# Optimization experiments

Hardware: AMD Instinct MI355X
Metric: run time of the kernel (lower is better)

Reference implementation:

```python
import jax, jax.numpy as jnp
import numpy as np

D_MODEL = 1024
NUM_HEADS = 16
D_HEAD = D_MODEL // NUM_HEADS
THETA = 10000.0


def _apply_rope(x, pos):
    # x: [B, H, S, Dh]; pos: [S]
    inv_freq = 1.0 / (THETA ** (jnp.arange(0, D_HEAD, 2, dtype=jnp.float32) / D_HEAD))  # [Dh/2]
    freqs = pos[:, None].astype(x.dtype) * inv_freq.astype(x.dtype)  # [S, Dh/2]
    cos = jnp.cos(freqs)  # [S, Dh/2]
    sin = jnp.sin(freqs)
    x1 = x[..., 0::2]  # [B, H, S, Dh/2]
    x2 = x[..., 1::2]
    even = x1 * cos - x2 * sin
    odd = x1 * sin + x2 * cos
    # interleave back: stack on last axis then flatten
    out = jnp.stack([even, odd], axis=-1).reshape(x.shape)
    return out


def setup_inputs() -> dict:
    key = jax.random.key(0)
    k0, k1, k2, k3, k4 = jax.random.split(key, 5)
    B, S = 2, 2048
    scale = 0.02
    return {
        "in_features": jax.random.normal(k0, (B, S, D_MODEL), dtype=jnp.float32),
        "Wq": jax.random.normal(k1, (D_MODEL, D_MODEL), dtype=jnp.float32) * scale,
        "Wk": jax.random.normal(k2, (D_MODEL, D_MODEL), dtype=jnp.float32) * scale,
        "Wv": jax.random.normal(k3, (D_MODEL, D_MODEL), dtype=jnp.float32) * scale,
        "Wo": jax.random.normal(k4, (D_MODEL, D_MODEL), dtype=jnp.float32) * scale,
    }


def reference(in_features, Wq, Wk, Wv, Wo):
    B, S, _ = in_features.shape
    H, Dh = NUM_HEADS, D_HEAD

    def proj(W):
        # torch Linear: y = x @ W^T; split heads -> [B, H, S, Dh]
        y = jnp.einsum('bsd,ed->bse', in_features, W)
        return y.reshape(B, S, H, Dh).transpose(0, 2, 1, 3)

    q = proj(Wq)
    k = proj(Wk)
    v = proj(Wv)

    pos = jnp.arange(S)
    q = _apply_rope(q, pos)
    k = _apply_rope(k, pos)

    scores = jnp.einsum('bhqd,bhkd->bhqk', q, k) / jnp.sqrt(jnp.asarray(Dh, q.dtype))
    causal = jnp.tril(jnp.ones((S, S), dtype=bool))  # True = keep
    scores = jnp.where(causal[None, None, :, :], scores, -jnp.inf)
    att = jax.nn.softmax(scores, axis=-1)
    out = jnp.einsum('bhqk,bhkd->bhqd', att, v)  # [B, H, S, Dh]
    out = out.transpose(0, 2, 1, 3).reshape(B, S, H * Dh)
    return jnp.einsum('bsd,ed->bse', out, Wo)
```

## Files before the change

kernel.cpp:

```cpp
#include <hip/hip_runtime.h>
#include <hip/hip_bf16.h>
#include <math.h>

#define D_MODEL 1024
#define NHEAD 16
#define DHEAD 64
#define SEQ 2048
#define BATCH 2
#define MTOT (BATCH * SEQ)

typedef __attribute__((ext_vector_type(8))) short bf16x8;
typedef __attribute__((ext_vector_type(4))) float f32x4;

static __device__ __forceinline__ ushort f2b(float x) {
  __hip_bfloat16 h = __float2bfloat16(x);
  union { __hip_bfloat16 h; ushort u; } cv; cv.h = h; return cv.u;
}

#define GLLDS16(gp, lp)                                                     \
  __builtin_amdgcn_global_load_lds(                                         \
      (const __attribute__((address_space(1))) unsigned int*)(gp),          \
      (__attribute__((address_space(3))) unsigned int*)(lp), 16, 0, 0)

#define QSCALE 0.18033688011112042f

__global__ __launch_bounds__(256)
void prep(const float* __restrict__ X, const float* __restrict__ Wq,
          const float* __restrict__ Wk, const float* __restrict__ Wv,
          const float* __restrict__ Wo, ushort* __restrict__ Xb,
          ushort* __restrict__ Wqb, ushort* __restrict__ Wkb,
          ushort* __restrict__ Wvb, ushort* __restrict__ Wob,
          float2* __restrict__ tbl) {
  int bid = blockIdx.x;
  if (bid >= 8192) {
    int idx = (bid - 8192) * 256 + threadIdx.x;
    int s = idx >> 5, i = idx & 31;
    float inv = exp2f((float)i * -0.4152410118609203f);
    float sn, cs;
    sincosf((float)s * inv, &sn, &cs);
    tbl[idx] = make_float2(cs, sn);
    return;
  }
  const float* in;
  ushort* out;
  int i;
  if (bid < 4096) {
    in = X; out = Xb; i = bid * 256 + threadIdx.x;
  } else {
    int ws = (bid - 4096) >> 10;
    in = (ws == 0) ? Wq : (ws == 1) ? Wk : (ws == 2) ? Wv : Wo;
    out = (ws == 0) ? Wqb : (ws == 1) ? Wkb : (ws == 2) ? Wvb : Wob;
    i = ((bid - 4096) & 1023) * 256 + threadIdx.x;
  }
  float4 v = ((const float4*)in)[i];
  ushort4 o;
  o.x = f2b(v.x); o.y = f2b(v.y); o.z = f2b(v.z); o.w = f2b(v.w);
  ((ushort4*)out)[i] = o;
}

__global__ __launch_bounds__(256)
void gemm_bf16(const ushort* __restrict__ A,
               const ushort* __restrict__ W0, const ushort* __restrict__ W1,
               const ushort* __restrict__ W2,
               const float2* __restrict__ tbl,
               float* __restrict__ outF,
               ushort* __restrict__ o0, ushort* __restrict__ o1,
               ushort* __restrict__ o2, int mode) {
  __shared__ ushort As[128 * 32];
  __shared__ ushort Bs[128 * 32];
  const int tid = threadIdx.x;
  const int lane = tid & 63;
  const int w = tid >> 6;
  const int quad = lane >> 4, l15 = lane & 15;
  const int wy = w >> 1, wx = w & 1;
  const int m0 = blockIdx.y * 128, n0 = blockIdx.x * 128;
  const int z = blockIdx.z;
  const ushort* W = (z == 0) ? W0 : (z == 1) ? W1 : W2;
  ushort* outB = (z == 0) ? o0 : (z == 1) ? o1 : o2;

  const int r0 = tid >> 2, c0 = tid & 3;
  const int gc = c0 ^ (((r0 >> 2) ^ r0) & 3);
  const ushort* Ag0 = A + (size_t)(m0 + r0) * D_MODEL + gc * 8;
  const ushort* Ag1 = A + (size_t)(m0 + r0 + 64) * D_MODEL + gc * 8;
  const ushort* Wg0 = W + (size_t)(n0 + r0) * D_MODEL + gc * 8;
  const ushort* Wg1 = W + (size_t)(n0 + r0 + 64) * D_MODEL + gc * 8;

  const int sw = (quad ^ (l15 >> 2) ^ l15) & 3;

  f32x4 acc[4][4];
#pragma unroll
  for (int i = 0; i < 4; ++i)
#pragma unroll
    for (int j = 0; j < 4; ++j) acc[i][j] = (f32x4){0.f, 0.f, 0.f, 0.f};

  for (int kt = 0; kt < D_MODEL / 32; ++kt) {
    if (kt) __syncthreads();
    GLLDS16(Ag0 + kt * 32, &As[(size_t)tid * 8]);
    GLLDS16(Ag1 + kt * 32, &As[(size_t)(tid + 256) * 8]);
    GLLDS16(Wg0 + kt * 32, &Bs[(size_t)tid * 8]);
    GLLDS16(Wg1 + kt * 32, &Bs[(size_t)(tid + 256) * 8]);
    __syncthreads();

    bf16x8 af[4], bfr[4];
#pragma unroll
    for (int mt = 0; mt < 4; ++mt) {
      int row = wy * 64 + mt * 16 + l15;
      af[mt] = *(const bf16x8*)&As[(row * 4 + sw) * 8];
    }
#pragma unroll
    for (int nt = 0; nt < 4; ++nt) {
      int row = wx * 64 + nt * 16 + l15;
      bfr[nt] = *(const bf16x8*)&Bs[(row * 4 + sw) * 8];
    }
#pragma unroll
    for (int mt = 0; mt < 4; ++mt)
#pragma unroll
      for (int nt = 0; nt < 4; ++nt)
        acc[mt][nt] = __builtin_amdgcn_mfma_f32_16x16x32_bf16(
            af[mt], bfr[nt], acc[mt][nt], 0, 0, 0);
  }

  const float qsc = (z == 0) ? QSCALE : 1.0f;
#pragma unroll
  for (int mt = 0; mt < 4; ++mt) {
    int m_base = m0 + wy * 64 + mt * 16 + quad * 4;
    int b = m_base >> 11, s_base = m_base & (SEQ - 1);
#pragma unroll
    for (int nt = 0; nt < 4; ++nt) {
      int n = n0 + wx * 64 + nt * 16 + l15;
      if (mode == 0) {
#pragma unroll
        for (int r = 0; r < 4; ++r)
          outF[(size_t)(m_base + r) * D_MODEL + n] = acc[mt][nt][r];
      } else {
        int h = n >> 6, dh = n & 63;
        if (z == 2) {
          int p_base = (s_base & ~31) | (((s_base >> 2) & 3) << 3) |
                       (((s_base >> 4) & 1) << 2);
          ushort4 o;
          o.x = f2b(acc[mt][nt][0]); o.y = f2b(acc[mt][nt][1]);
          o.z = f2b(acc[mt][nt][2]); o.w = f2b(acc[mt][nt][3]);
          *(ushort4*)&outB[((size_t)(b * NHEAD + h) * DHEAD + dh) * SEQ + p_base] = o;
        } else {
          int i = nt * 8 + (l15 >> 1);
          bool evn = !(l15 & 1);
#pragma unroll
          for (int r = 0; r < 4; ++r) {
            float v = acc[mt][nt][r];
            float pv = __shfl_xor(v, 1);
            float2 csn = tbl[(s_base + r) * 32 + i];
            v = v * csn.x + (evn ? -pv * csn.y : pv * csn.y);
            v *= qsc;
            outB[(((size_t)(b * NHEAD + h)) * SEQ + s_base + r) * DHEAD + dh] = f2b(v);
          }
        }
      }
    }
  }
}

__global__ __launch_bounds__(256)
void flash_mfma(const ushort* __restrict__ Q, const ushort* __restrict__ K,
                const ushort* __restrict__ Vt, ushort* __restrict__ O) {
  __shared__ ushort Ks[64 * 64];
  __shared__ ushort Vs[64 * 64];
  const int tid = threadIdx.x;
  const int lane = tid & 63, w = tid >> 6;
  const int quad = lane >> 4, l15 = lane & 15;
  const int h = blockIdx.y, b = blockIdx.z;
  const int qt = (h >= 8) ? (31 - blockIdx.x) : blockIdx.x;
  const int bh = b * NHEAD + h;

  const int qrow = qt * 64 + w * 16 + l15;
  const ushort* Qrow = Q + ((size_t)bh * SEQ + qrow) * 64;
  bf16x8 aq0 = *(const bf16x8*)(Qrow + quad * 8);
  bf16x8 aq1 = *(const bf16x8*)(Qrow + 32 + quad * 8);

  const int rl = tid >> 3;
  const int gsc = (tid & 7) ^ (rl & 7);
  const ushort* Kg0 = K + ((size_t)bh * SEQ + rl) * 64 + gsc * 8;
  const ushort* Kg1 = Kg0 + (size_t)32 * 64;
  const ushort* Vg0 = Vt + ((size_t)bh * 64 + rl) * SEQ + gsc * 8;
  const ushort* Vg1 = Vg0 + (size_t)32 * SEQ;

  const int sA = (quad ^ (l15 & 7)) * 8;
  const int sB = sA ^ 32;

  float rsl = 0.f;
  f32x4 accO[4];
#pragma unroll
  for (int nt = 0; nt < 4; ++nt) accO[nt] = (f32x4){0.f, 0.f, 0.f, 0.f};

  float4 pk0 = *(const float4*)(Kg0);
  float4 pk1 = *(const float4*)(Kg1);
  float4 pv0 = *(const float4*)(Vg0);
  float4 pv1 = *(const float4*)(Vg1);

  for (int kt = 0; kt <= qt; ++kt) {
    __syncthreads();
    *(float4*)&Ks[tid * 8]        = pk0;
    *(float4*)&Ks[2048 + tid * 8] = pk1;
    *(float4*)&Vs[tid * 8]        = pv0;
    *(float4*)&Vs[2048 + tid * 8] = pv1;
    __syncthreads();
    if (kt < qt) {
      pk0 = *(const float4*)(Kg0 + (size_t)(kt + 1) * 64 * 64);
      pk1 = *(const float4*)(Kg1 + (size_t)(kt + 1) * 64 * 64);
      pv0 = *(const float4*)(Vg0 + (kt + 1) * 64);
      pv1 = *(const float4*)(Vg1 + (kt + 1) * 64);
    }

    f32x4 sc[4];
#pragma unroll
    for (int nt = 0; nt < 4; ++nt) {
      const ushort* kr = &Ks[(nt * 16 + l15) * 64];
      bf16x8 bk0 = *(const bf16x8*)(kr + sA);
      bf16x8 bk1 = *(const bf16x8*)(kr + sB);
      f32x4 zz = (f32x4){0.f, 0.f, 0.f, 0.f};
      zz = __builtin_amdgcn_mfma_f32_16x16x32_bf16(bk0, aq0, zz, 0, 0, 0);
      zz = __builtin_amdgcn_mfma_f32_16x16x32_bf16(bk1, aq1, zz, 0, 0, 0);
      sc[nt] = zz;
    }

    const bool diag = (kt == qt);
    uint pk[8];
#pragma unroll
    for (int nt = 0; nt < 4; ++nt) {
      int kbase = kt * 64 + nt * 16 + quad * 4;
      ushort us[4];
#pragma unroll
      for (int r = 0; r < 4; ++r) {
        float p = __builtin_amdgcn_exp2f(sc[nt][r]);
        if (diag && kbase + r > qrow) p = 0.f;
        rsl += p;
        us[r] = f2b(p);
      }
      pk[nt * 2]     = (uint)us[0] | ((uint)us[1] << 16);
      pk[nt * 2 + 1] = (uint)us[2] | ((uint)us[3] << 16);
    }
    union { uint u[4]; bf16x8 v; } B0, B1;
    B0.u[0] = pk[0]; B0.u[1] = pk[1]; B0.u[2] = pk[2]; B0.u[3] = pk[3];
    B1.u[0] = pk[4]; B1.u[1] = pk[5]; B1.u[2] = pk[6]; B1.u[3] = pk[7];

#pragma unroll
    for (int nt = 0; nt < 4; ++nt) {
      const ushort* vr = &Vs[(nt * 16 + l15) * 64];
      bf16x8 av0 = *(const bf16x8*)(vr + sA);
      bf16x8 av1 = *(const bf16x8*)(vr + sB);
      accO[nt] = __builtin_amdgcn_mfma_f32_16x16x32_bf16(av0, B0.v, accO[nt], 0, 0, 0);
      accO[nt] = __builtin_amdgcn_mfma_f32_16x16x32_bf16(av1, B1.v, accO[nt], 0, 0, 0);
    }
  }

  rsl += __shfl_xor(rsl, 16);
  rsl += __shfl_xor(rsl, 32);
  float invl = 1.f / rsl;

  size_t base = ((size_t)(b * SEQ + qrow)) * D_MODEL + h * 64;
#pragma unroll
  for (int nt = 0; nt < 4; ++nt) {
    ushort4 o;
    o.x = f2b(accO[nt][0] * invl);
    o.y = f2b(accO[nt][1] * invl);
    o.z = f2b(accO[nt][2] * invl);
    o.w = f2b(accO[nt][3] * invl);
    *(ushort4*)&O[base + nt * 16 + quad * 4] = o;
  }
}

extern "C" void kernel_launch(void* const* d_in, const int* in_sizes, int n_in,
                              void* d_out, int out_size, void* d_ws, size_t ws_size,
                              hipStream_t stream) {
  const float* X  = (const float*)d_in[0];
  const float* Wq = (const float*)d_in[1];
  const float* Wk = (const float*)d_in[2];
  const float* Wv = (const float*)d_in[3];
  const float* Wo = (const float*)d_in[4];
  float* out = (float*)d_out;

  ushort* Xb  = (ushort*)d_ws;
  ushort* Wqb = Xb  + (size_t)MTOT * D_MODEL;
  ushort* Wkb = Wqb + (size_t)D_MODEL * D_MODEL;
  ushort* Wvb = Wkb + (size_t)D_MODEL * D_MODEL;
  ushort* Wob = Wvb + (size_t)D_MODEL * D_MODEL;
  ushort* Qw  = Wob + (size_t)D_MODEL * D_MODEL;
  ushort* Kw  = Qw  + (size_t)MTOT * D_MODEL;
  ushort* Vtw = Kw  + (size_t)MTOT * D_MODEL;
  ushort* At  = Vtw + (size_t)MTOT * D_MODEL;
  float2* tbl = (float2*)(At + (size_t)MTOT * D_MODEL);

  prep<<<8448, 256, 0, stream>>>(X, Wq, Wk, Wv, Wo, Xb, Wqb, Wkb, Wvb, Wob, tbl);

  gemm_bf16<<<dim3(D_MODEL / 128, MTOT / 128, 3), 256, 0, stream>>>(
      Xb, Wqb, Wkb, Wvb, tbl, nullptr, Qw, Kw, Vtw, 1);

  flash_mfma<<<dim3(SEQ / 64, NHEAD, BATCH), 256, 0, stream>>>(Qw, Kw, Vtw, At);

  gemm_bf16<<<dim3(D_MODEL / 128, MTOT / 128, 1), 256, 0, stream>>>(
      At, Wob, nullptr, nullptr, tbl, out, nullptr, nullptr, nullptr, 0);
}
```

Measured before the change: 173.4 us.

## Add 256x256-tile pipelined QKV GEMM kernel with swizzled LDS and block remap

Replaces the 128x128 QKV projection GEMM with a new 512-thread kernel that computes 256x256 output tiles. It stages A and B through 128 KB of double-buffered, XOR-swizzled LDS using direct global-to-LDS loads, with explicit waitcnt and barrier choreography and setprio around the MFMA bursts. It also remaps block indices for L2 locality. The goal is more data reuse per tile and better overlap of loads with MFMA work. The cost is only 192 blocks, which may leave CUs idle, plus heavy LDS use and a fragile hand-written sync schedule.

Result: slower. 178.4 us (+2.9%).

```diff
diff --git a/kernel.cpp b/kernel.cpp
--- a/kernel.cpp
+++ b/kernel.cpp
@@ -23,6 +23,25 @@
       (__attribute__((address_space(3))) unsigned int*)(lp), 16, 0, 0)
 
 #define QSCALE 0.18033688011112042f
+
+#define MFMA16(a_, b_, c_) \
+  __builtin_amdgcn_mfma_f32_16x16x32_bf16(a_, b_, c_, 0, 0, 0)
+#define SBAR() __builtin_amdgcn_s_barrier()
+#define WAIT_LGKM0                                         \
+  do {                                                     \
+    asm volatile("s_waitcnt lgkmcnt(0)" ::: "memory");     \
+    __builtin_amdgcn_sched_barrier(0);                     \
+  } while (0)
+#define WAIT_VM6                                           \
+  do {                                                     \
+    asm volatile("s_waitcnt vmcnt(6)" ::: "memory");       \
+    __builtin_amdgcn_sched_barrier(0);                     \
+  } while (0)
+#define WAIT_VM0                                           \
+  do {                                                     \
+    asm volatile("s_waitcnt vmcnt(0)" ::: "memory");       \
+    __builtin_amdgcn_sched_barrier(0);                     \
+  } while (0)
 
 __global__ __launch_bounds__(256)
 void prep(const float* __restrict__ X, const float* __restrict__ Wq,
@@ -56,6 +75,180 @@
   ushort4 o;
   o.x = f2b(v.x); o.y = f2b(v.y); o.z = f2b(v.z); o.w = f2b(v.w);
   ((ushort4*)out)[i] = o;
+}
+
+__global__ __launch_bounds__(512, 2)
+void gemm256_qkv(const ushort* __restrict__ A,
+                 const ushort* __restrict__ W0, const ushort* __restrict__ W1,
+                 const ushort* __restrict__ W2,
+                 const float2* __restrict__ tbl,
+                 ushort* __restrict__ o0, ushort* __restrict__ o1,
+                 ushort* __restrict__ o2) {
+  __shared__ ushort sm[65536];
+  const int tid = threadIdx.x;
+  const int lane = tid & 63;
+  const int w = tid >> 6;
+  const int wy = w >> 2, wx = w & 3;
+  const int quad = lane >> 4, l15 = lane & 15;
+
+  int flat = blockIdx.x + (blockIdx.y << 2) + (blockIdx.z << 6);
+  int nf = (flat & 7) * 24 + (flat >> 3);
+  const int z = nf >> 6;
+  const int m0 = ((nf >> 2) & 15) << 8;
+  const int n0 = (nf & 3) << 8;
+
+  const ushort* W = (z == 0) ? W0 : (z == 1) ? W1 : W2;
+  ushort* outB = (z == 0) ? o0 : (z == 1) ? o1 : o2;
+
+  const int sr = tid >> 3;
+  const int scx = (tid & 7) ^ (sr & 7);
+  const ushort* Ag = A + (size_t)(m0 + sr) * D_MODEL + scx * 8;
+  const ushort* Wg = W + (size_t)(n0 + sr) * D_MODEL + scx * 8;
+
+#define STG_A(u, h)                                                         \
+  do {                                                                      \
+    GLLDS16(Ag + (size_t)((h) * 128) * D_MODEL + (u) * 64,                  \
+            &sm[((u) & 1) * 16384 + (h) * 8192 + tid * 8]);                 \
+    GLLDS16(Ag + (size_t)((h) * 128 + 64) * D_MODEL + (u) * 64,             \
+            &sm[((u) & 1) * 16384 + (h) * 8192 + 4096 + tid * 8]);          \
+  } while (0)
+#define STG_B(u, h)                                                         \
+  do {                                                                      \
+    GLLDS16(Wg + (size_t)((h) * 128) * D_MODEL + (u) * 64,                  \
+            &sm[32768 + ((u) & 1) * 16384 + (h) * 8192 + tid * 8]);         \
+    GLLDS16(Wg + (size_t)((h) * 128 + 64) * D_MODEL + (u) * 64,             \
+            &sm[32768 + ((u) & 1) * 16384 + (h) * 8192 + 4096 + tid * 8]);  \
+  } while (0)
+
+  const int slot0 = quad ^ (l15 & 7);
+  const int aoff = (wy * 64 + l15) * 64 + slot0 * 8;
+  const int boff = (wx * 32 + l15) * 64 + slot0 * 8;
+
+  f32x4 acc[8][4];
+#pragma unroll
+  for (int i = 0; i < 8; ++i)
+#pragma unroll
+    for (int j = 0; j < 4; ++j) acc[i][j] = (f32x4){0.f, 0.f, 0.f, 0.f};
+
+  bf16x8 a[4][2], bl[2][2], bh[2][2];
+
+  STG_A(0, 0); STG_B(0, 0); STG_B(0, 1); STG_A(0, 1);
+  STG_A(1, 0); STG_B(1, 0); STG_B(1, 1);
+  WAIT_VM6;
+  SBAR();
+
+  for (int u = 0; u < 16; ++u) {
+    const ushort* As_ = &sm[(u & 1) * 16384];
+    const ushort* Bs_ = &sm[32768 + (u & 1) * 16384];
+
+#pragma unroll
+    for (int i = 0; i < 4; ++i) {
+      a[i][0] = *(const bf16x8*)&As_[aoff + i * 1024];
+      a[i][1] = *(const bf16x8*)&As_[(aoff ^ 32) + i * 1024];
+    }
+#pragma unroll
+    for (int j = 0; j < 2; ++j) {
+      bl[j][0] = *(const bf16x8*)&Bs_[boff + j * 1024];
+      bl[j][1] = *(const bf16x8*)&Bs_[(boff ^ 32) + j * 1024];
+    }
+    if (u < 15) STG_A(u + 1, 1);
+    SBAR();
+    WAIT_LGKM0;
+    __builtin_amdgcn_s_setprio(1);
+#pragma unroll
+    for (int i = 0; i < 4; ++i)
+#pragma unroll
+      for (int j = 0; j < 2; ++j) {
+        acc[i][j] = MFMA16(a[i][0], bl[j][0], acc[i][j]);
+        acc[i][j] = MFMA16(a[i][1], bl[j][1], acc[i][j]);
+      }
+    __builtin_amdgcn_s_setprio(0);
+    SBAR();
+
+#pragma unroll
+    for (int j = 0; j < 2; ++j) {
+      bh[j][0] = *(const bf16x8*)&Bs_[8192 + boff + j * 1024];
+      bh[j][1] = *(const bf16x8*)&Bs_[8192 + (boff ^ 32) + j * 1024];
+    }
+    if (u < 14) STG_A(u + 2, 0);
+    SBAR();
+    WAIT_LGKM0;
+    __builtin_amdgcn_s_setprio(1);
+#pragma unroll
+    for (int i = 0; i < 4; ++i)
+#pragma unroll
+      for (int j = 0; j < 2; ++j) {
+        acc[i][2 + j] = MFMA16(a[i][0], bh[j][0], acc[i][2 + j]);
+        acc[i][2 + j] = MFMA16(a[i][1], bh[j][1], acc[i][2 + j]);
+      }
+    __builtin_amdgcn_s_setprio(0);
+    SBAR();
+
+#pragma unroll
+    for (int i = 0; i < 4; ++i) {
+      a[i][0] = *(const bf16x8*)&As_[8192 + aoff + i * 1024];
+      a[i][1] = *(const bf16x8*)&As_[8192 + (aoff ^ 32) + i * 1024];
+    }
+    if (u < 14) STG_B(u + 2, 0);
+    SBAR();
+    WAIT_LGKM0;
+    __builtin_amdgcn_s_setprio(1);
+#pragma unroll
+    for (int i = 0; i < 4; ++i)
+#pragma unroll
+      for (int j = 0; j < 2; ++j) {
+        acc[4 + i][j] = MFMA16(a[i][0], bl[j][0], acc[4 + i][j]);
+        acc[4 + i][j] = MFMA16(a[i][1], bl[j][1], acc[4 + i][j]);
+      }
+    __builtin_amdgcn_s_setprio(0);
+    SBAR();
+
+    if (u < 14) STG_B(u + 2, 1);
+    SBAR();
+    __builtin_amdgcn_s_setprio(1);
+#pragma unroll
+    for (int i = 0; i < 4; ++i)
+#pragma unroll
+      for (int j = 0; j < 2; ++j) {
+        acc[4 + i][2 + j] = MFMA16(a[i][0], bh[j][0], acc[4 + i][2 + j]);
+        acc[4 + i][2 + j] = MFMA16(a[i][1], bh[j][1], acc[4 + i][2 + j]);
+      }
+    __builtin_amdgcn_s_setprio(0);
+    if (u < 14) { WAIT_VM6; } else { WAIT_VM0; }
+    SBAR();
+  }
+
+  const float qsc = (z == 0) ? QSCALE : 1.0f;
+#pragma unroll
+  for (int mt = 0; mt < 8; ++mt) {
+    int gm = m0 + ((mt >> 2) << 7) + wy * 64 + (mt & 3) * 16 + quad * 4;
+    int b = gm >> 11, s_base = gm & (SEQ - 1);
+#pragma unroll
+    for (int nt = 0; nt < 4; ++nt) {
+      int n = n0 + ((nt >> 1) << 7) + wx * 32 + (nt & 1) * 16 + l15;
+      int h = n >> 6, dh = n & 63;
+      if (z == 2) {
+        int p_base = (s_base & ~31) | (((s_base >> 2) & 3) << 3) |
+                     (((s_base >> 4) & 1) << 2);
+        ushort4 o;
+        o.x = f2b(acc[mt][nt][0]); o.y = f2b(acc[mt][nt][1]);
+        o.z = f2b(acc[mt][nt][2]); o.w = f2b(acc[mt][nt][3]);
+        *(ushort4*)&outB[((size_t)(b * NHEAD + h) * DHEAD + dh) * SEQ + p_base] = o;
+      } else {
+        int fi = dh >> 1;
+        bool evn = !(dh & 1);
+#pragma unroll
+        for (int r = 0; r < 4; ++r) {
+          float v = acc[mt][nt][r];
+          float pv = __shfl_xor(v, 1);
+          float2 csn = tbl[(s_base + r) * 32 + fi];
+          v = v * csn.x + (evn ? -pv * csn.y : pv * csn.y);
+          v *= qsc;
+          outB[(((size_t)(b * NHEAD + h)) * SEQ + s_base + r) * DHEAD + dh] = f2b(v);
+        }
+      }
+    }
+  }
 }
 
 __global__ __launch_bounds__(256)
@@ -291,8 +484,8 @@
 
   prep<<<8448, 256, 0, stream>>>(X, Wq, Wk, Wv, Wo, Xb, Wqb, Wkb, Wvb, Wob, tbl);
 
-  gemm_bf16<<<dim3(D_MODEL / 128, MTOT / 128, 3), 256, 0, stream>>>(
-      Xb, Wqb, Wkb, Wvb, tbl, nullptr, Qw, Kw, Vtw, 1);
+  gemm256_qkv<<<dim3(D_MODEL / 256, MTOT / 256, 3), 512, 0, stream>>>(
+      Xb, Wqb, Wkb, Wvb, tbl, Qw, Kw, Vtw);
 
   flash_mfma<<<dim3(SEQ / 64, NHEAD, BATCH), 256, 0, stream>>>(Qw, Kw, Vtw, At);
 
```

## Process two adjacent query tiles per flash block to reuse K/V tiles

Applied to the files above, without the earlier changes.

Each flash attention block now handles two consecutive 64-row query tiles (ta, tb) and shares every K/V tile it loads into shared memory between both, skipping the lower tile's work once past its diagonal. This halves the grid, roughly halving redundant K/V global loads and LDS staging. In exchange register pressure doubles (two accumulator sets and two Q fragments), and a launch-bounds hint of 2 blocks per CU is added. The smaller grid of 512 blocks may reduce occupancy and load balance.

Result: slower. 190.1 us (+9.6%).

```diff
diff --git a/kernel.cpp b/kernel.cpp
--- a/kernel.cpp
+++ b/kernel.cpp
@@ -159,7 +159,7 @@
   }
 }
 
-__global__ __launch_bounds__(256)
+__global__ __launch_bounds__(256, 2)
 void flash_mfma(const ushort* __restrict__ Q, const ushort* __restrict__ K,
                 const ushort* __restrict__ Vt, ushort* __restrict__ O) {
   __shared__ ushort Ks[64 * 64];
@@ -168,13 +168,18 @@
   const int lane = tid & 63, w = tid >> 6;
   const int quad = lane >> 4, l15 = lane & 15;
   const int h = blockIdx.y, b = blockIdx.z;
-  const int qt = (h >= 8) ? (31 - blockIdx.x) : blockIdx.x;
+  const int tp = (h >= 8) ? (15 - blockIdx.x) : blockIdx.x;
+  const int ta = 2 * tp, tb = 2 * tp + 1;
   const int bh = b * NHEAD + h;
 
-  const int qrow = qt * 64 + w * 16 + l15;
-  const ushort* Qrow = Q + ((size_t)bh * SEQ + qrow) * 64;
-  bf16x8 aq0 = *(const bf16x8*)(Qrow + quad * 8);
-  bf16x8 aq1 = *(const bf16x8*)(Qrow + 32 + quad * 8);
+  const int qrowA = ta * 64 + w * 16 + l15;
+  const int qrowB = tb * 64 + w * 16 + l15;
+  const ushort* QrA = Q + ((size_t)bh * SEQ + qrowA) * 64;
+  const ushort* QrB = Q + ((size_t)bh * SEQ + qrowB) * 64;
+  bf16x8 aqA0 = *(const bf16x8*)(QrA + quad * 8);
+  bf16x8 aqA1 = *(const bf16x8*)(QrA + 32 + quad * 8);
+  bf16x8 aqB0 = *(const bf16x8*)(QrB + quad * 8);
+  bf16x8 aqB1 = *(const bf16x8*)(QrB + 32 + quad * 8);
 
   const int rl = tid >> 3;
   const int gsc = (tid & 7) ^ (rl & 7);
@@ -186,85 +191,129 @@
   const int sA = (quad ^ (l15 & 7)) * 8;
   const int sB = sA ^ 32;
 
-  float rsl = 0.f;
-  f32x4 accO[4];
-#pragma unroll
-  for (int nt = 0; nt < 4; ++nt) accO[nt] = (f32x4){0.f, 0.f, 0.f, 0.f};
+  float rslA = 0.f, rslB = 0.f;
+  f32x4 accA[4], accB[4];
+#pragma unroll
+  for (int nt = 0; nt < 4; ++nt) {
+    accA[nt] = (f32x4){0.f, 0.f, 0.f, 0.f};
+    accB[nt] = (f32x4){0.f, 0.f, 0.f, 0.f};
+  }
 
   float4 pk0 = *(const float4*)(Kg0);
   float4 pk1 = *(const float4*)(Kg1);
   float4 pv0 = *(const float4*)(Vg0);
   float4 pv1 = *(const float4*)(Vg1);
 
-  for (int kt = 0; kt <= qt; ++kt) {
+  for (int kt = 0; kt <= tb; ++kt) {
     __syncthreads();
     *(float4*)&Ks[tid * 8]        = pk0;
     *(float4*)&Ks[2048 + tid * 8] = pk1;
     *(float4*)&Vs[tid * 8]        = pv0;
     *(float4*)&Vs[2048 + tid * 8] = pv1;
     __syncthreads();
-    if (kt < qt) {
+    if (kt < tb) {
       pk0 = *(const float4*)(Kg0 + (size_t)(kt + 1) * 64 * 64);
       pk1 = *(const float4*)(Kg1 + (size_t)(kt + 1) * 64 * 64);
       pv0 = *(const float4*)(Vg0 + (kt + 1) * 64);
       pv1 = *(const float4*)(Vg1 + (kt + 1) * 64);
     }
-
-    f32x4 sc[4];
+    const bool gA = (kt <= ta);
+
+    f32x4 scA[4], scB[4];
 #pragma unroll
     for (int nt = 0; nt < 4; ++nt) {
       const ushort* kr = &Ks[(nt * 16 + l15) * 64];
       bf16x8 bk0 = *(const bf16x8*)(kr + sA);
       bf16x8 bk1 = *(const bf16x8*)(kr + sB);
-      f32x4 zz = (f32x4){0.f, 0.f, 0.f, 0.f};
-      zz = __builtin_amdgcn_mfma_f32_16x16x32_bf16(bk0, aq0, zz, 0, 0, 0);
-      zz = __builtin_amdgcn_mfma_f32_16x16x32_bf16(bk1, aq1, zz, 0, 0, 0);
-      sc[nt] = zz;
-    }
-
-    const bool diag = (kt == qt);
-    uint pk[8];
+      f32x4 zb = (f32x4){0.f, 0.f, 0.f, 0.f};
+      zb = __builtin_amdgcn_mfma_f32_16x16x32_bf16(bk0, aqB0, zb, 0, 0, 0);
+      zb = __builtin_amdgcn_mfma_f32_16x16x32_bf16(bk1, aqB1, zb, 0, 0, 0);
+      scB[nt] = zb;
+      if (gA) {
+        f32x4 za = (f32x4){0.f, 0.f, 0.f, 0.f};
+        za = __builtin_amdgcn_mfma_f32_16x16x32_bf16(bk0, aqA0, za, 0, 0, 0);
+        za = __builtin_amdgcn_mfma_f32_16x16x32_bf16(bk1, aqA1, za, 0, 0, 0);
+        scA[nt] = za;
+      }
+    }
+
+    const bool diagB = (kt == tb);
+    uint pkB[8];
 #pragma unroll
     for (int nt = 0; nt < 4; ++nt) {
       int kbase = kt * 64 + nt * 16 + quad * 4;
       ushort us[4];
 #pragma unroll
       for (int r = 0; r < 4; ++r) {
-        float p = __builtin_amdgcn_exp2f(sc[nt][r]);
-        if (diag && kbase + r > qrow) p = 0.f;
-        rsl += p;
+        float p = __builtin_amdgcn_exp2f(scB[nt][r]);
+        if (diagB && kbase + r > qrowB) p = 0.f;
+        rslB += p;
         us[r] = f2b(p);
       }
-      pk[nt * 2]     = (uint)us[0] | ((uint)us[1] << 16);
-      pk[nt * 2 + 1] = (uint)us[2] | ((uint)us[3] << 16);
-    }
-    union { uint u[4]; bf16x8 v; } B0, B1;
-    B0.u[0] = pk[0]; B0.u[1] = pk[1]; B0.u[2] = pk[2]; B0.u[3] = pk[3];
-    B1.u[0] = pk[4]; B1.u[1] = pk[5]; B1.u[2] = pk[6]; B1.u[3] = pk[7];
+      pkB[nt * 2]     = (uint)us[0] | ((uint)us[1] << 16);
+      pkB[nt * 2 + 1] = (uint)us[2] | ((uint)us[3] << 16);
+    }
+    union { uint u[4]; bf16x8 v; } BB0, BB1, BA0, BA1;
+    BB0.u[0] = pkB[0]; BB0.u[1] = pkB[1]; BB0.u[2] = pkB[2]; BB0.u[3] = pkB[3];
+    BB1.u[0] = pkB[4]; BB1.u[1] = pkB[5]; BB1.u[2] = pkB[6]; BB1.u[3] = pkB[7];
+
+    if (gA) {
+      const bool diagA = (kt == ta);
+      uint pkA[8];
+#pragma unroll
+      for (int nt = 0; nt < 4; ++nt) {
+        int kbase = kt * 64 + nt * 16 + quad * 4;
+        ushort us[4];
+#pragma unroll
+        for (int r = 0; r < 4; ++r) {
+          float p = __builtin_amdgcn_exp2f(scA[nt][r]);
+          if (diagA && kbase + r > qrowA) p = 0.f;
+          rslA += p;
+          us[r] = f2b(p);
+        }
+        pkA[nt * 2]     = (uint)us[0] | ((uint)us[1] << 16);
+        pkA[nt * 2 + 1] = (uint)us[2] | ((uint)us[3] << 16);
+      }
+      BA0.u[0] = pkA[0]; BA0.u[1] = pkA[1]; BA0.u[2] = pkA[2]; BA0.u[3] = pkA[3];
+      BA1.u[0] = pkA[4]; BA1.u[1] = pkA[5]; BA1.u[2] = pkA[6]; BA1.u[3] = pkA[7];
+    }
 
 #pragma unroll
     for (int nt = 0; nt < 4; ++nt) {
       const ushort* vr = &Vs[(nt * 16 + l15) * 64];
       bf16x8 av0 = *(const bf16x8*)(vr + sA);
       bf16x8 av1 = *(const bf16x8*)(vr + sB);
-      accO[nt] = __builtin_amdgcn_mfma_f32_16x16x32_bf16(av0, B0.v, accO[nt], 0, 0, 0);
-      accO[nt] = __builtin_amdgcn_mfma_f32_16x16x32_bf16(av1, B1.v, accO[nt], 0, 0, 0);
-    }
-  }
-
-  rsl += __shfl_xor(rsl, 16);
-  rsl += __shfl_xor(rsl, 32);
-  float invl = 1.f / rsl;
-
-  size_t base = ((size_t)(b * SEQ + qrow)) * D_MODEL + h * 64;
+      accB[nt] = __builtin_amdgcn_mfma_f32_16x16x32_bf16(av0, BB0.v, accB[nt], 0, 0, 0);
+      accB[nt] = __builtin_amdgcn_mfma_f32_16x16x32_bf16(av1, BB1.v, accB[nt], 0, 0, 0);
+      if (gA) {
+        accA[nt] = __builtin_amdgcn_mfma_f32_16x16x32_bf16(av0, BA0.v, accA[nt], 0, 0, 0);
+        accA[nt] = __builtin_amdgcn_mfma_f32_16x16x32_bf16(av1, BA1.v, accA[nt], 0, 0, 0);
+      }
+    }
+  }
+
+  rslA += __shfl_xor(rslA, 16);
+  rslA += __shfl_xor(rslA, 32);
+  rslB += __shfl_xor(rslB, 16);
+  rslB += __shfl_xor(rslB, 32);
+  float invA = 1.f / rslA;
+  float invB = 1.f / rslB;
+
+  size_t baseA = ((size_t)(b * SEQ + qrowA)) * D_MODEL + h * 64;
+  size_t baseB = ((size_t)(b * SEQ + qrowB)) * D_MODEL + h * 64;
 #pragma unroll
   for (int nt = 0; nt < 4; ++nt) {
-    ushort4 o;
-    o.x = f2b(accO[nt][0] * invl);
-    o.y = f2b(accO[nt][1] * invl);
-    o.z = f2b(accO[nt][2] * invl);
-    o.w = f2b(accO[nt][3] * invl);
-    *(ushort4*)&O[base + nt * 16 + quad * 4] = o;
+    ushort4 oa, ob;
+    oa.x = f2b(accA[nt][0] * invA);
+    oa.y = f2b(accA[nt][1] * invA);
+    oa.z = f2b(accA[nt][2] * invA);
+    oa.w = f2b(accA[nt][3] * invA);
+    *(ushort4*)&O[baseA + nt * 16 + quad * 4] = oa;
+    ob.x = f2b(accB[nt][0] * invB);
+    ob.y = f2b(accB[nt][1] * invB);
+    ob.z = f2b(accB[nt][2] * invB);
+    ob.w = f2b(accB[nt][3] * invB);
+    *(ushort4*)&O[baseB + nt * 16 + quad * 4] = ob;
   }
 }
 
@@ -294,7 +343,7 @@
   gemm_bf16<<<dim3(D_MODEL / 128, MTOT / 128, 3), 256, 0, stream>>>(
       Xb, Wqb, Wkb, Wvb, tbl, nullptr, Qw, Kw, Vtw, 1);
 
-  flash_mfma<<<dim3(SEQ / 64, NHEAD, BATCH), 256, 0, stream>>>(Qw, Kw, Vtw, At);
+  flash_mfma<<<dim3(SEQ / 128, NHEAD, BATCH), 256, 0, stream>>>(Qw, Kw, Vtw, At);
 
   gemm_bf16<<<dim3(D_MODEL / 128, MTOT / 128, 1), 256, 0, stream>>>(
       At, Wob, nullptr, nullptr, tbl, out, nullptr, nullptr, nullptr, 0);
```

## Load K/V directly from global in flash kernel, remap grid for XCD locality

Applied to the files above, without the earlier changes.

Removes the shared-memory staging of K and V tiles and their two barriers per iteration; each wave now loads its MFMA operands for K and V straight from global memory. The 3D grid becomes a 1D grid with a block-index remap that places all query tiles of one (batch, head) on the same XCD (bid & 7) for L2 reuse, and the launch-bounds hint now asks for 4 blocks per SM. In exchange, each of the four waves reads the same K/V tile redundantly from cache, and there is no explicit prefetch to hide global latency.

After: 368.9 us. +112.8%, slower.

```diff
diff --git a/kernel.cpp b/kernel.cpp
--- a/kernel.cpp
+++ b/kernel.cpp
@@ -159,63 +159,48 @@
   }
 }
 
-__global__ __launch_bounds__(256)
+__global__ __launch_bounds__(256, 4)
 void flash_mfma(const ushort* __restrict__ Q, const ushort* __restrict__ K,
                 const ushort* __restrict__ Vt, ushort* __restrict__ O) {
-  __shared__ ushort Ks[64 * 64];
-  __shared__ ushort Vs[64 * 64];
   const int tid = threadIdx.x;
   const int lane = tid & 63, w = tid >> 6;
   const int quad = lane >> 4, l15 = lane & 15;
-  const int h = blockIdx.y, b = blockIdx.z;
-  const int qt = (h >= 8) ? (31 - blockIdx.x) : blockIdx.x;
-  const int bh = b * NHEAD + h;
+
+  const int bid = blockIdx.x;
+  const int i = bid >> 3;
+  const int g = (bid & 7) * 4 + (i >> 5);
+  const int h = g & (NHEAD - 1);
+  int qt = i & 31;
+  if (h >= 8) qt = 31 - qt;
+  const int bh = g;
 
   const int qrow = qt * 64 + w * 16 + l15;
   const ushort* Qrow = Q + ((size_t)bh * SEQ + qrow) * 64;
   bf16x8 aq0 = *(const bf16x8*)(Qrow + quad * 8);
   bf16x8 aq1 = *(const bf16x8*)(Qrow + 32 + quad * 8);
 
-  const int rl = tid >> 3;
-  const int gsc = (tid & 7) ^ (rl & 7);
-  const ushort* Kg0 = K + ((size_t)bh * SEQ + rl) * 64 + gsc * 8;
-  const ushort* Kg1 = Kg0 + (size_t)32 * 64;
-  const ushort* Vg0 = Vt + ((size_t)bh * 64 + rl) * SEQ + gsc * 8;
-  const ushort* Vg1 = Vg0 + (size_t)32 * SEQ;
-
-  const int sA = (quad ^ (l15 & 7)) * 8;
-  const int sB = sA ^ 32;
+  const ushort* Kp0 = K + ((size_t)bh * SEQ + l15) * 64 + quad * 8;
+  const ushort* Vp0 = Vt + ((size_t)bh * 64 + l15) * SEQ + quad * 8;
 
   float rsl = 0.f;
   f32x4 accO[4];
 #pragma unroll
   for (int nt = 0; nt < 4; ++nt) accO[nt] = (f32x4){0.f, 0.f, 0.f, 0.f};
 
-  float4 pk0 = *(const float4*)(Kg0);
-  float4 pk1 = *(const float4*)(Kg1);
-  float4 pv0 = *(const float4*)(Vg0);
-  float4 pv1 = *(const float4*)(Vg1);
-
   for (int kt = 0; kt <= qt; ++kt) {
-    __syncthreads();
-    *(float4*)&Ks[tid * 8]        = pk0;
-    *(float4*)&Ks[2048 + tid * 8] = pk1;
-    *(float4*)&Vs[tid * 8]        = pv0;
-    *(float4*)&Vs[2048 + tid * 8] = pv1;
-    __syncthreads();
-    if (kt < qt) {
-      pk0 = *(const float4*)(Kg0 + (size_t)(kt + 1) * 64 * 64);
-      pk1 = *(const float4*)(Kg1 + (size_t)(kt + 1) * 64 * 64);
-      pv0 = *(const float4*)(Vg0 + (kt + 1) * 64);
-      pv1 = *(const float4*)(Vg1 + (kt + 1) * 64);
-    }
-
+    const ushort* Kt = Kp0 + (size_t)kt * 64 * 64;
+    const ushort* Vc = Vp0 + kt * 64;
+
+    bf16x8 av0[4], av1[4];
     f32x4 sc[4];
 #pragma unroll
     for (int nt = 0; nt < 4; ++nt) {
-      const ushort* kr = &Ks[(nt * 16 + l15) * 64];
-      bf16x8 bk0 = *(const bf16x8*)(kr + sA);
-      bf16x8 bk1 = *(const bf16x8*)(kr + sB);
+      const ushort* kp = Kt + nt * (16 * 64);
+      const ushort* vp = Vc + (size_t)nt * (16 * SEQ);
+      bf16x8 bk0 = *(const bf16x8*)kp;
+      bf16x8 bk1 = *(const bf16x8*)(kp + 32);
+      av0[nt] = *(const bf16x8*)vp;
+      av1[nt] = *(const bf16x8*)(vp + 32);
       f32x4 zz = (f32x4){0.f, 0.f, 0.f, 0.f};
       zz = __builtin_amdgcn_mfma_f32_16x16x32_bf16(bk0, aq0, zz, 0, 0, 0);
       zz = __builtin_amdgcn_mfma_f32_16x16x32_bf16(bk1, aq1, zz, 0, 0, 0);
@@ -244,11 +229,8 @@
 
 #pragma unroll
     for (int nt = 0; nt < 4; ++nt) {
-      const ushort* vr = &Vs[(nt * 16 + l15) * 64];
-      bf16x8 av0 = *(const bf16x8*)(vr + sA);
-      bf16x8 av1 = *(const bf16x8*)(vr + sB);
-      accO[nt] = __builtin_amdgcn_mfma_f32_16x16x32_bf16(av0, B0.v, accO[nt], 0, 0, 0);
-      accO[nt] = __builtin_amdgcn_mfma_f32_16x16x32_bf16(av1, B1.v, accO[nt], 0, 0, 0);
+      accO[nt] = __builtin_amdgcn_mfma_f32_16x16x32_bf16(av0[nt], B0.v, accO[nt], 0, 0, 0);
+      accO[nt] = __builtin_amdgcn_mfma_f32_16x16x32_bf16(av1[nt], B1.v, accO[nt], 0, 0, 0);
     }
   }
 
@@ -256,6 +238,7 @@
   rsl += __shfl_xor(rsl, 32);
   float invl = 1.f / rsl;
 
+  const int b = g >> 4;
   size_t base = ((size_t)(b * SEQ + qrow)) * D_MODEL + h * 64;
 #pragma unroll
   for (int nt = 0; nt < 4; ++nt) {
@@ -294,7 +277,7 @@
   gemm_bf16<<<dim3(D_MODEL / 128, MTOT / 128, 3), 256, 0, stream>>>(
       Xb, Wqb, Wkb, Wvb, tbl, nullptr, Qw, Kw, Vtw, 1);
 
-  flash_mfma<<<dim3(SEQ / 64, NHEAD, BATCH), 256, 0, stream>>>(Qw, Kw, Vtw, At);
+  flash_mfma<<<dim3(SEQ / 64 * NHEAD * BATCH), 256, 0, stream>>>(Qw, Kw, Vtw, At);
 
   gemm_bf16<<<dim3(D_MODEL / 128, MTOT / 128, 1), 256, 0, stream>>>(
       At, Wob, nullptr, nullptr, tbl, out, nullptr, nullptr, nullptr, 0);
```
